# Kernel tuning notes

Hardware: AMD Instinct MI355X
Metric: run time of the kernel (lower is better)

The kernel has to match this reference:

```python
import jax, jax.numpy as jnp
import numpy as np
import math

N_HEADS = 12
ROPE_DIM = 64
BASE = 10000.0


def _rope_tables(seq_len, dim):
    inv_freq = 1.0 / (BASE ** (jnp.arange(0, dim, 2, dtype=jnp.float32) / dim))
    t = jnp.arange(seq_len, dtype=jnp.float32)
    freqs = jnp.outer(t, inv_freq)                      # [S, dim/2]
    emb = jnp.concatenate([freqs, freqs], axis=-1)      # [S, dim]
    # broadcast shape [1, S, 1, dim]
    return jnp.cos(emb)[None, :, None, :], jnp.sin(emb)[None, :, None, :]


def _rotate_half(x):
    x1, x2 = jnp.split(x, 2, axis=-1)
    return jnp.concatenate([-x2, x1], axis=-1)


def setup_inputs() -> dict:
    key = jax.random.key(0)
    ks = jax.random.split(key, 9)
    B, S, E = 2, 2048, 768
    s = 1.0 / math.sqrt(E)
    return {
        "x": jax.random.normal(ks[0], (B, S, E), jnp.float32),
        "Wq": jax.random.normal(ks[1], (E, E), jnp.float32) * s,
        "bq": jax.random.normal(ks[2], (E,), jnp.float32) * 0.02,
        "Wk": jax.random.normal(ks[3], (E, E), jnp.float32) * s,
        "bk": jax.random.normal(ks[4], (E,), jnp.float32) * 0.02,
        "Wv": jax.random.normal(ks[5], (E, E), jnp.float32) * s,
        "bv": jax.random.normal(ks[6], (E,), jnp.float32) * 0.02,
        "Wp": jax.random.normal(ks[7], (E, E), jnp.float32) * s,
        "bp": jax.random.normal(ks[8], (E,), jnp.float32) * 0.02,
    }


def reference(x, Wq, bq, Wk, bk, Wv, bv, Wp, bp):
    B, S, E = x.shape
    H = N_HEADS
    D = E // H

    q = (x @ Wq + bq).reshape(B, S, H, D)
    k = (x @ Wk + bk).reshape(B, S, H, D)
    v = (x @ Wv + bv).reshape(B, S, H, D)

    # rotary on first ROPE_DIM dims (here ROPE_DIM == D, so full rotary)
    cos, sin = _rope_tables(S, ROPE_DIM)
    q_rot, q_pass = q[..., :ROPE_DIM], q[..., ROPE_DIM:]
    k_rot, k_pass = k[..., :ROPE_DIM], k[..., ROPE_DIM:]
    q_rot = q_rot * cos + _rotate_half(q_rot) * sin
    k_rot = k_rot * cos + _rotate_half(k_rot) * sin
    q = jnp.concatenate([q_rot, q_pass], axis=-1)
    k = jnp.concatenate([k_rot, k_pass], axis=-1)

    # scores [B, M, N, H]; mask before scaling (as in the torch code; -inf unchanged)
    att = jnp.einsum("bmhd,bnhd->bmnh", q, k)
    causal = jnp.tril(jnp.ones((S, S), dtype=bool))[None, :, :, None]
    att = jnp.where(causal, att, -jnp.inf)
    att = jax.nn.softmax(att / math.sqrt(D), axis=2)
    out = jnp.einsum("bmnh,bnhd->bmhd", att, v)

    return out.reshape(B, S, E) @ Wp + bp
```

## Files before the change

kernel.cpp:

```cpp
#include <hip/hip_runtime.h>
#include <stdint.h>

#define S_LEN 2048
#define EMB   768
#define NH    12
#define DH    64
#define M_TOT 4096
#define WELEM 589824
#define QELEM 3145728

typedef float  floatx4 __attribute__((ext_vector_type(4)));
typedef __bf16 bf16x8  __attribute__((ext_vector_type(8)));
typedef __bf16 bf16x4  __attribute__((ext_vector_type(4)));
typedef unsigned short ushortx4 __attribute__((ext_vector_type(4)));

__device__ __forceinline__ unsigned short f2bf(float f) {
    union { float f; unsigned u; } v; v.f = f;
    unsigned u = v.u;
    unsigned r = (u + 0x7FFFu + ((u >> 16) & 1u)) >> 16;
    return (unsigned short)r;
}

__device__ __forceinline__ void gl_lds16(const void* g, void* l) {
    __builtin_amdgcn_global_load_lds(
        (__attribute__((address_space(1))) const void*)g,
        (__attribute__((address_space(3))) void*)l, 16, 0, 0);
}

__global__ void cvt_all_kernel(const float* __restrict__ x, unsigned short* __restrict__ xb,
                               const float* __restrict__ W0, const float* __restrict__ W1,
                               const float* __restrict__ W2, const float* __restrict__ W3,
                               unsigned short* __restrict__ WT_all, float2* __restrict__ rope) {
    __shared__ float t[64][65];
    const int blk = blockIdx.x;
    if (blk < 3072) {
        int i = (blk * 256 + threadIdx.x) * 4;
        float4 v = *(const float4*)(x + i);
        ushortx4 r = { f2bf(v.x), f2bf(v.y), f2bf(v.z), f2bf(v.w) };
        *(ushortx4*)(xb + i) = r;
        return;
    }
    if (blk >= 3648) {
        int idx = (blk - 3648) * 256 + threadIdx.x;
        int s = idx >> 5, d = idx & 31;
        float f = exp2f((float)d * -0.41524101186092034f);
        float th = (float)s * f;
        float sn, cs; sincosf(th, &sn, &cs);
        rope[idx] = make_float2(cs, sn);
        return;
    }
    const int tc = blk - 3072;
    const int z = tc / 144, rr0 = tc % 144;
    const float* W = (z == 0) ? W0 : (z == 1 ? W1 : (z == 2 ? W2 : W3));
    unsigned short* O = WT_all + (size_t)z * WELEM;
    const int k0 = (rr0 % 12) * 64, n0 = (rr0 / 12) * 64;
    const int c = threadIdx.x & 63, r4 = threadIdx.x >> 6;
#pragma unroll
    for (int rr = 0; rr < 64; rr += 4) {
        int r = rr + r4;
        t[r][c] = W[(size_t)(k0 + r) * EMB + n0 + c];
    }
    __syncthreads();
#pragma unroll
    for (int rr = 0; rr < 64; rr += 4) {
        int nn = rr + r4;
        O[(size_t)(n0 + nn) * EMB + k0 + c] = f2bf(t[c][nn]);
    }
}

static __device__ __forceinline__ void gemm_core_128x128(
    const unsigned short* __restrict__ A, const unsigned short* __restrict__ BT,
    int m0, int n0, int K, int tid, floatx4 (&acc)[4][4],
    unsigned short* Als, unsigned short* Bls)
{
    const int lane = tid & 63;
    const int c0 = lane & 15, quad = lane >> 4;
    const int wave = tid >> 6;
    const int wm = (wave >> 1) * 64, wn = (wave & 1) * 64;

    for (int k0 = 0; k0 < K; k0 += 64) {
        __syncthreads();
#pragma unroll
        for (int it = 0; it < 4; ++it) {
            int ch = it * 256 + tid;
            int row = ch >> 3, sc = ch & 7;
            int cc = sc ^ (row & 7);
            gl_lds16(A  + (size_t)(m0 + row) * K + k0 + cc * 8, Als + ch * 8);
            gl_lds16(BT + (size_t)(n0 + row) * K + k0 + cc * 8, Bls + ch * 8);
        }
        __syncthreads();
        bf16x8 af[4][2], bfv[4][2];
#pragma unroll
        for (int ii = 0; ii < 4; ++ii) {
            int row = wm + 16 * ii + c0;
#pragma unroll
            for (int h = 0; h < 2; ++h)
                af[ii][h] = *(const bf16x8*)(Als + row * 64 + (((4 * h + quad) ^ (row & 7)) * 8));
        }
#pragma unroll
        for (int jj = 0; jj < 4; ++jj) {
            int row = wn + 16 * jj + c0;
#pragma unroll
            for (int h = 0; h < 2; ++h)
                bfv[jj][h] = *(const bf16x8*)(Bls + row * 64 + (((4 * h + quad) ^ (row & 7)) * 8));
        }
#pragma unroll
        for (int ii = 0; ii < 4; ++ii)
#pragma unroll
            for (int jj = 0; jj < 4; ++jj) {
                acc[ii][jj] = __builtin_amdgcn_mfma_f32_16x16x32_bf16(af[ii][0], bfv[jj][0], acc[ii][jj], 0, 0, 0);
                acc[ii][jj] = __builtin_amdgcn_mfma_f32_16x16x32_bf16(af[ii][1], bfv[jj][1], acc[ii][jj], 0, 0, 0);
            }
    }
}

__global__ __launch_bounds__(256, 2) void qkv_kernel(
    const unsigned short* __restrict__ xb, const unsigned short* __restrict__ WT_all,
    const float* __restrict__ bq, const float* __restrict__ bk, const float* __restrict__ bv,
    const float2* __restrict__ rope, unsigned short* __restrict__ qkv_out)
{
    __shared__ __align__(16) unsigned short Als[128 * 64];
    __shared__ __align__(16) unsigned short Bls[128 * 64];
    const int z = blockIdx.z;
    const float* bias = (z == 0) ? bq : (z == 1 ? bk : bv);
    __bf16* Cout = (__bf16*)(qkv_out + (size_t)z * QELEM);
    const int m0 = blockIdx.x * 128, n0 = blockIdx.y * 128;
    const int tid = threadIdx.x, lane = tid & 63, c0 = lane & 15, quad = lane >> 4, wave = tid >> 6;
    const int wm = (wave >> 1) * 64, wn = (wave & 1) * 64;

    floatx4 acc[4][4] = {};
    gemm_core_128x128(xb, WT_all + (size_t)z * WELEM, m0, n0, EMB, tid, acc, Als, Bls);

    if (z == 2) {
#pragma unroll
        for (int ii = 0; ii < 4; ++ii) {
            int m = m0 + wm + 16 * ii + quad * 4;
            int b = m >> 11, s = m & (S_LEN - 1);
#pragma unroll
            for (int jj = 0; jj < 4; ++jj) {
                int n = n0 + wn + 16 * jj + c0;
                int h = n >> 6, d = n & 63;
                float bn = bias[n];
                bf16x4 pv;
#pragma unroll
                for (int r = 0; r < 4; ++r) pv[r] = (__bf16)(acc[ii][jj][r] + bn);
                *(bf16x4*)(Cout + ((size_t)(b * NH + h) * DH + d) * S_LEN + s) = pv;
            }
        }
        return;
    }

#pragma unroll
    for (int ii = 0; ii < 4; ++ii) {
#pragma unroll
        for (int r = 0; r < 4; ++r) {
            int m = m0 + wm + 16 * ii + quad * 4 + r;
            int b = m >> 11, s = m & (S_LEN - 1);
            float vals[4];
#pragma unroll
            for (int jj = 0; jj < 4; ++jj) vals[jj] = acc[ii][jj][r] + bias[n0 + wn + 16 * jj + c0];
#pragma unroll
            for (int jj = 0; jj < 2; ++jj) {
                int d = 16 * jj + c0;
                float2 t = rope[s * 32 + d];
                float lo = vals[jj], hi = vals[jj + 2];
                vals[jj]     = lo * t.x - hi * t.y;
                vals[jj + 2] = hi * t.x + lo * t.y;
            }
            if (z == 0) {
#pragma unroll
                for (int jj = 0; jj < 4; ++jj) vals[jj] *= 0.18033688011112042f;
            }
#pragma unroll
            for (int jj = 0; jj < 4; ++jj) {
                int n = n0 + wn + 16 * jj + c0;
                int h = n >> 6, d = n & 63;
                Cout[((size_t)(b * NH + h) * S_LEN + s) * DH + d] = (__bf16)vals[jj];
            }
        }
    }
}

__global__ __launch_bounds__(256, 3) void flash_kernel(
    const unsigned short* __restrict__ Qg, const unsigned short* __restrict__ Kg,
    const unsigned short* __restrict__ Vt, unsigned short* __restrict__ Og)
{
    __shared__ __align__(16) unsigned short Kls[2][64 * 64];
    __shared__ __align__(16) unsigned short Vls[2][64 * 64];
    __shared__ __align__(16) unsigned short Pls[4][16 * 72];

    const int i = blockIdx.x;
    const int kk = i >> 8, g = i & 255;
    const int r0 = (kk == 0) ? g : (kk == 1 ? 511 - g : 512 + g);
    const int qt = 31 - r0 / 24;
    const int bh = r0 % 24;
    const int b = bh / NH, h = bh % NH;
    const int m0 = qt * 64;
    const int tid = threadIdx.x, lane = tid & 63, wave = tid >> 6;
    const int c0 = lane & 15, quad = lane >> 4;
    const size_t base = (size_t)bh * S_LEN * DH;
    const int mrow = m0 + wave * 16 + c0;

    bf16x8 qf0 = *(const bf16x8*)(Qg + base + (size_t)mrow * DH + quad * 8);
    bf16x8 qf1 = *(const bf16x8*)(Qg + base + (size_t)mrow * DH + 32 + quad * 8);

    floatx4 oa[4] = {};
    float l_lane = 0.f;
    const float C = 23.083120654223414f;
    const int ntiles = qt + 1;

#pragma unroll
    for (int it = 0; it < 2; ++it) {
        int ch = it * 256 + tid;
        int row = ch >> 3, cc = (ch & 7) ^ (row & 7);
        gl_lds16(Kg + base + (size_t)row * DH + cc * 8, &Kls[0][ch * 8]);
        gl_lds16(Vt + base + (size_t)row * S_LEN + cc * 8, &Vls[0][ch * 8]);
    }

    for (int nt = 0; nt < ntiles; ++nt) {
        __syncthreads();
        if (nt + 1 < ntiles) {
            int n0 = (nt + 1) * 64, buf = (nt + 1) & 1;
#pragma unroll
            for (int it = 0; it < 2; ++it) {
                int ch = it * 256 + tid;
                int row = ch >> 3, cc = (ch & 7) ^ (row & 7);
                gl_lds16(Kg + base + (size_t)(n0 + row) * DH + cc * 8, &Kls[buf][ch * 8]);
                gl_lds16(Vt + base + (size_t)row * S_LEN + n0 + cc * 8, &Vls[buf][ch * 8]);
            }
        }
        const unsigned short* Kb = Kls[nt & 1];
        const unsigned short* Vb = Vls[nt & 1];

        floatx4 sa[4];
        const floatx4 zz = { 0.f, 0.f, 0.f, 0.f };
        __builtin_amdgcn_s_setprio(1);
#pragma unroll
        for (int jj = 0; jj < 4; ++jj) {
            int row = 16 * jj + c0;
            bf16x8 k0 = *(const bf16x8*)(Kb + row * 64 + ((quad ^ (row & 7)) * 8));
            bf16x8 k1 = *(const bf16x8*)(Kb + row * 64 + (((4 + quad) ^ (row & 7)) * 8));
            sa[jj] = __builtin_amdgcn_mfma_f32_16x16x32_bf16(k0, qf0, zz, 0, 0, 0);
            sa[jj] = __builtin_amdgcn_mfma_f32_16x16x32_bf16(k1, qf1, sa[jj], 0, 0, 0);
        }
        __builtin_amdgcn_s_setprio(0);
        if (nt == ntiles - 1) {
#pragma unroll
            for (int jj = 0; jj < 4; ++jj) {
                int nb = m0 + 16 * jj + quad * 4;
#pragma unroll
                for (int rr = 0; rr < 4; ++rr)
                    if (nb + rr > mrow) sa[jj][rr] = -1e30f;
            }
        }
#pragma unroll
        for (int jj = 0; jj < 4; ++jj) {
            bf16x4 pw;
#pragma unroll
            for (int rr = 0; rr < 4; ++rr) {
                float p = __builtin_amdgcn_exp2f(sa[jj][rr] - C);
                l_lane += p;
                pw[rr] = (__bf16)p;
            }
            *(bf16x4*)(&Pls[wave][c0 * 72 + 16 * jj + quad * 4]) = pw;
        }
        __builtin_amdgcn_s_setprio(1);
#pragma unroll
        for (int h2 = 0; h2 < 2; ++h2) {
            bf16x8 pf = *(const bf16x8*)(&Pls[wave][c0 * 72 + 32 * h2 + quad * 8]);
#pragma unroll
            for (int dt = 0; dt < 4; ++dt) {
                int row = 16 * dt + c0;
                bf16x8 vf = *(const bf16x8*)(Vb + row * 64 + (((4 * h2 + quad) ^ (row & 7)) * 8));
                oa[dt] = __builtin_amdgcn_mfma_f32_16x16x32_bf16(vf, pf, oa[dt], 0, 0, 0);
            }
        }
        __builtin_amdgcn_s_setprio(0);
    }

    l_lane += __shfl_xor(l_lane, 16, 64);
    l_lane += __shfl_xor(l_lane, 32, 64);
    const float rl = 1.0f / l_lane;
    __bf16* Ob16 = (__bf16*)Og;
#pragma unroll
    for (int dt = 0; dt < 4; ++dt) {
        bf16x4 ov;
#pragma unroll
        for (int rr = 0; rr < 4; ++rr) ov[rr] = (__bf16)(oa[dt][rr] * rl);
        *(bf16x4*)(Ob16 + ((size_t)(b * S_LEN + mrow)) * EMB + h * DH + dt * 16 + quad * 4) = ov;
    }
}

__global__ __launch_bounds__(256, 2) void proj_kernel(
    const unsigned short* __restrict__ Ob, const unsigned short* __restrict__ WpT,
    const float* __restrict__ bp, float* __restrict__ out)
{
    __shared__ __align__(16) unsigned short Als[128 * 64];
    __shared__ __align__(16) unsigned short Bls[128 * 64];
    const int m0 = blockIdx.x * 128, n0 = blockIdx.y * 128;
    const int tid = threadIdx.x, lane = tid & 63, c0 = lane & 15, quad = lane >> 4, wave = tid >> 6;
    const int wm = (wave >> 1) * 64, wn = (wave & 1) * 64;

    floatx4 acc[4][4] = {};
    gemm_core_128x128(Ob, WpT, m0, n0, EMB, tid, acc, Als, Bls);

#pragma unroll
    for (int ii = 0; ii < 4; ++ii)
#pragma unroll
        for (int r = 0; r < 4; ++r) {
            int m = m0 + wm + 16 * ii + quad * 4 + r;
#pragma unroll
            for (int jj = 0; jj < 4; ++jj) {
                int n = n0 + wn + 16 * jj + c0;
                out[(size_t)m * EMB + n] = acc[ii][jj][r] + bp[n];
            }
        }
}

extern "C" void kernel_launch(void* const* d_in, const int* in_sizes, int n_in,
                              void* d_out, int out_size, void* d_ws, size_t ws_size,
                              hipStream_t stream)
{
    (void)in_sizes; (void)n_in; (void)out_size;
    const float* x  = (const float*)d_in[0];
    const float* Wq = (const float*)d_in[1];
    const float* bq = (const float*)d_in[2];
    const float* Wk = (const float*)d_in[3];
    const float* bk = (const float*)d_in[4];
    const float* Wv = (const float*)d_in[5];
    const float* bv = (const float*)d_in[6];
    const float* Wp = (const float*)d_in[7];
    const float* bp = (const float*)d_in[8];

    unsigned short* ws  = (unsigned short*)d_ws;
    unsigned short* xb  = ws;
    unsigned short* WT  = xb + (size_t)QELEM;
    unsigned short* QKV = WT + 4 * (size_t)WELEM;
    unsigned short* Ob  = QKV + 3 * (size_t)QELEM;
    float2* rope = (float2*)(Ob + (size_t)QELEM);
    if (ws_size < ((size_t)QELEM * 5 + 4 * (size_t)WELEM) * 2 + 2048 * 32 * 8) return;

    cvt_all_kernel<<<3904, 256, 0, stream>>>(x, xb, Wq, Wk, Wv, Wp, WT, rope);
    qkv_kernel<<<dim3(32, 6, 3), 256, 0, stream>>>(xb, WT, bq, bk, bv, (const float2*)rope, QKV);
    flash_kernel<<<dim3(768), 256, 0, stream>>>(QKV, QKV + QELEM, QKV + 2 * (size_t)QELEM, Ob);
    proj_kernel<<<dim3(32, 6), 256, 0, stream>>>(Ob, WT + 3 * (size_t)WELEM, bp, (float*)d_out);
}
```

Baseline: 155.6 us.

## Triple-buffer K/V tiles in flash kernel with explicit vmcnt waits, retune launch bounds

The flash attention kernel moves from double to triple buffering of K/V tiles in LDS. It prefetches two tiles ahead and replaces __syncthreads with an explicit s_waitcnt vmcnt plus s_barrier, so loads for the next tiles can stay in flight across the barrier. Launch bounds change too: flash drops to 2 blocks per SM to make room for the extra LDS, and the qkv and proj GEMM kernels go up to 3. This trades occupancy for deeper memory latency hiding. The hand-counted vmcnt also depends on how the compiler orders the loads.

Measured after the change: 156.1 us. About the same (+0.3%).

```diff
diff --git a/kernel.cpp b/kernel.cpp
--- a/kernel.cpp
+++ b/kernel.cpp
@@ -114,7 +114,7 @@
     }
 }
 
-__global__ __launch_bounds__(256, 2) void qkv_kernel(
+__global__ __launch_bounds__(256, 3) void qkv_kernel(
     const unsigned short* __restrict__ xb, const unsigned short* __restrict__ WT_all,
     const float* __restrict__ bq, const float* __restrict__ bk, const float* __restrict__ bv,
     const float2* __restrict__ rope, unsigned short* __restrict__ qkv_out)
@@ -181,12 +181,12 @@
     }
 }
 
-__global__ __launch_bounds__(256, 3) void flash_kernel(
+__global__ __launch_bounds__(256, 2) void flash_kernel(
     const unsigned short* __restrict__ Qg, const unsigned short* __restrict__ Kg,
     const unsigned short* __restrict__ Vt, unsigned short* __restrict__ Og)
 {
-    __shared__ __align__(16) unsigned short Kls[2][64 * 64];
-    __shared__ __align__(16) unsigned short Vls[2][64 * 64];
+    __shared__ __align__(16) unsigned short Kls[3][64 * 64];
+    __shared__ __align__(16) unsigned short Vls[3][64 * 64];
     __shared__ __align__(16) unsigned short Pls[4][16 * 72];
 
     const int i = blockIdx.x;
@@ -203,34 +203,40 @@
 
     bf16x8 qf0 = *(const bf16x8*)(Qg + base + (size_t)mrow * DH + quad * 8);
     bf16x8 qf1 = *(const bf16x8*)(Qg + base + (size_t)mrow * DH + 32 + quad * 8);
+    asm volatile("" :: "v"(qf0), "v"(qf1));
 
     floatx4 oa[4] = {};
     float l_lane = 0.f;
     const float C = 23.083120654223414f;
     const int ntiles = qt + 1;
 
-#pragma unroll
-    for (int it = 0; it < 2; ++it) {
-        int ch = it * 256 + tid;
-        int row = ch >> 3, cc = (ch & 7) ^ (row & 7);
-        gl_lds16(Kg + base + (size_t)row * DH + cc * 8, &Kls[0][ch * 8]);
-        gl_lds16(Vt + base + (size_t)row * S_LEN + cc * 8, &Vls[0][ch * 8]);
-    }
+#define STAGE_TILE(T, BUF)                                                              \
+    {                                                                                   \
+        _Pragma("unroll")                                                               \
+        for (int it = 0; it < 2; ++it) {                                                \
+            int ch = it * 256 + tid;                                                    \
+            int row = ch >> 3, cc = (ch & 7) ^ (row & 7);                               \
+            gl_lds16(Kg + base + (size_t)((T) * 64 + row) * DH + cc * 8,                \
+                     &Kls[BUF][ch * 8]);                                                \
+            gl_lds16(Vt + base + (size_t)row * S_LEN + (T) * 64 + cc * 8,               \
+                     &Vls[BUF][ch * 8]);                                                \
+        }                                                                               \
+    }
+
+    STAGE_TILE(0, 0);
+    if (ntiles > 1) STAGE_TILE(1, 1);
 
     for (int nt = 0; nt < ntiles; ++nt) {
-        __syncthreads();
-        if (nt + 1 < ntiles) {
-            int n0 = (nt + 1) * 64, buf = (nt + 1) & 1;
-#pragma unroll
-            for (int it = 0; it < 2; ++it) {
-                int ch = it * 256 + tid;
-                int row = ch >> 3, cc = (ch & 7) ^ (row & 7);
-                gl_lds16(Kg + base + (size_t)(n0 + row) * DH + cc * 8, &Kls[buf][ch * 8]);
-                gl_lds16(Vt + base + (size_t)row * S_LEN + n0 + cc * 8, &Vls[buf][ch * 8]);
-            }
-        }
-        const unsigned short* Kb = Kls[nt & 1];
-        const unsigned short* Vb = Vls[nt & 1];
+        const int buf = nt % 3;
+        if (nt + 1 < ntiles) asm volatile("s_waitcnt vmcnt(4)" ::: "memory");
+        else                 asm volatile("s_waitcnt vmcnt(0)" ::: "memory");
+        __builtin_amdgcn_s_barrier();
+        asm volatile("" ::: "memory");
+        if (nt + 2 < ntiles) {
+            STAGE_TILE(nt + 2, (nt + 2) % 3);
+        }
+        const unsigned short* Kb = Kls[buf];
+        const unsigned short* Vb = Vls[buf];
 
         floatx4 sa[4];
         const floatx4 zz = { 0.f, 0.f, 0.f, 0.f };
@@ -277,6 +283,7 @@
         }
         __builtin_amdgcn_s_setprio(0);
     }
+#undef STAGE_TILE
 
     l_lane += __shfl_xor(l_lane, 16, 64);
     l_lane += __shfl_xor(l_lane, 32, 64);
@@ -291,7 +298,7 @@
     }
 }
 
-__global__ __launch_bounds__(256, 2) void proj_kernel(
+__global__ __launch_bounds__(256, 3) void proj_kernel(
     const unsigned short* __restrict__ Ob, const unsigned short* __restrict__ WpT,
     const float* __restrict__ bp, float* __restrict__ out)
 {
```
